# Kernel tuning notes

Measured on AMD Instinct MI355X. Metric: run time of the kernel, lower is better.

## Reference

```python
import jax, jax.numpy as jnp
import numpy as np

BETA = 0.9      # membrane decay
THRESH = 1.0    # firing threshold


def _lif(x):
    """Leaky integrate-and-fire over leading time axis. x: (T, ..., C) -> spikes (T, ..., C)."""
    def step(mem, xt):
        mem = BETA * mem + xt
        s = (mem > THRESH).astype(xt.dtype)
        mem = mem - s * THRESH  # soft reset
        return mem, s
    _, spikes = jax.lax.scan(step, jnp.zeros_like(x[0]), x)
    return spikes


def setup_inputs() -> dict:
    key = jax.random.key(0)
    k1, k2, k3, k4, k5 = jax.random.split(key, 5)
    T, N, D = 4, 8192, 1024
    E, EF, TOPK = 8, 512, 2  # expert_ff = d_ff // n_experts = 4096 // 8
    x = jax.random.normal(k1, (T, N, D), dtype=jnp.float32)
    expert_indices = jax.random.randint(k2, (N, TOPK), 0, E)
    expert_weights = jax.random.uniform(k3, (N, TOPK), dtype=jnp.float32)
    up_w = jax.random.normal(k4, (E, EF, D), dtype=jnp.float32) * 0.02   # Linear(d_model, ef).weight
    down_w = jax.random.normal(k5, (E, D, EF), dtype=jnp.float32) * 0.02  # Linear(ef, d_model).weight
    return {"x": x, "expert_indices": expert_indices, "expert_weights": expert_weights,
            "up_w": up_w, "down_w": down_w}


def reference(x, expert_indices, expert_weights, up_w, down_w):
    T, N, D = x.shape
    E = up_w.shape[0]
    # Dense combine weights W[n, e] = sum_k weights[n, k] * (indices[n, k] == e)
    W = jnp.zeros((N, E), dtype=x.dtype).at[
        jnp.arange(N)[:, None], expert_indices].add(expert_weights)
    out = jnp.zeros_like(x)
    for e in range(E):  # fixed small loop over experts
        h = _lif(jnp.einsum('tnd,fd->tnf', x, up_w[e]))   # up-proj + LIF hidden
        o = _lif(jnp.einsum('tnf,df->tnd', h, down_w[e]))  # down-proj + LIF output
        out = out + o * W[:, e][None, :, None]             # weighted combine (0 for inactive)
    return out
```

## Files before the change

### kernel.cpp

```cpp
#include <hip/hip_runtime.h>
#include <stdint.h>

#define T_STEPS 4
#define NTOK    8192
#define DMODEL  1024
#define NEXP    8
#define EFF     512
#define BMT     128
#define CAPTOT  (2*NTOK + NEXP*BMT)

typedef __attribute__((ext_vector_type(8))) short bf8_t;
typedef __attribute__((ext_vector_type(4))) float f32x4;

#define MFMA(a,b,c) __builtin_amdgcn_mfma_f32_16x16x32_bf16((a),(b),(c),0,0,0)

#define SWZC(r, c) ((((c) ^ (((r) >> 1) & 3))) * 8)


__device__ __forceinline__ unsigned short bf16rn(float f) {
    unsigned u = __float_as_uint(f);
    unsigned r = u + 0x7fffu + ((u >> 16) & 1u);
    return (unsigned short)(r >> 16);
}
__device__ __forceinline__ float bf2f(unsigned short h) {
    return __uint_as_float(((unsigned)h) << 16);
}
__device__ __forceinline__ unsigned pk(unsigned short a, unsigned short b) {
    return (unsigned)a | ((unsigned)b << 16);
}

__device__ __forceinline__ void split8v(float4 va, float4 vb,
                                        unsigned short* d0, unsigned short* d1,
                                        unsigned short* d2) {
    float v[8];
    *(float4*)&v[0] = va;
    *(float4*)&v[4] = vb;
    unsigned short h[8], m[8], l[8];
#pragma unroll
    for (int i = 0; i < 8; ++i) {
        unsigned short a = bf16rn(v[i]);
        float r1 = v[i] - bf2f(a);
        unsigned short b = bf16rn(r1);
        float r2 = r1 - bf2f(b);
        h[i] = a; m[i] = b; l[i] = bf16rn(r2);
    }
    *(uint4*)d0 = make_uint4(pk(h[0],h[1]), pk(h[2],h[3]), pk(h[4],h[5]), pk(h[6],h[7]));
    *(uint4*)d1 = make_uint4(pk(m[0],m[1]), pk(m[2],m[3]), pk(m[4],m[5]), pk(m[6],m[7]));
    *(uint4*)d2 = make_uint4(pk(l[0],l[1]), pk(l[2],l[3]), pk(l[4],l[5]), pk(l[6],l[7]));
}

__device__ __forceinline__ void stage8_3limb(const float* __restrict__ src,
                                             unsigned short* d0, unsigned short* d1,
                                             unsigned short* d2) {
    float4 va = *(const float4*)(src + 0);
    float4 vb = *(const float4*)(src + 4);
    split8v(va, vb, d0, d1, d2);
}


__global__ void k_split(const float* __restrict__ w, unsigned short* __restrict__ h,
                        unsigned short* __restrict__ m, unsigned short* __restrict__ l) {
    size_t i = (size_t)(blockIdx.x * blockDim.x + threadIdx.x) * 8;
    stage8_3limb(w + i, h + i, m + i, l + i);
}


__global__ void k_count(const int* __restrict__ idx, int* __restrict__ counts) {
    int n = blockIdx.x * blockDim.x + threadIdx.x;
    if (n >= NTOK) return;
    int e0 = idx[2*n], e1 = idx[2*n+1];
    atomicAdd(&counts[e0], 1);
    if (e1 != e0) atomicAdd(&counts[e1], 1);
}

__global__ void k_prefix(const int* __restrict__ counts, int* __restrict__ offsets) {
    if (threadIdx.x == 0) {
        int o = 0;
        for (int e = 0; e < NEXP; ++e) {
            offsets[e] = o;
            o += (counts[e] + BMT - 1) / BMT * BMT;
        }
        offsets[NEXP] = o;
    }
}

__global__ void k_fill(const int* __restrict__ idx, const float* __restrict__ wts,
                       const int* __restrict__ offsets, int* __restrict__ cursors,
                       int* __restrict__ tok, float* __restrict__ wgt) {
    int n = blockIdx.x * blockDim.x + threadIdx.x;
    if (n >= NTOK) return;
    int e0 = idx[2*n], e1 = idx[2*n+1];
    float w0 = wts[2*n], w1 = wts[2*n+1];
    if (e0 == e1) w0 = __fadd_rn(w0, w1);
    int p0 = offsets[e0] + atomicAdd(&cursors[e0], 1);
    tok[p0] = n; wgt[p0] = w0;
    if (e1 != e0) {
        int p1 = offsets[e1] + atomicAdd(&cursors[e1], 1);
        tok[p1] = n; wgt[p1] = w1;
    }
}


__global__ __launch_bounds__(256, 2)
void k_up(const float* __restrict__ x,
          const unsigned short* __restrict__ uwh, const unsigned short* __restrict__ uwm,
          const unsigned short* __restrict__ uwl,
          const int* __restrict__ offsets, const int* __restrict__ tok,
          unsigned short* __restrict__ spk) {
    const int m0 = blockIdx.x * BMT;
    const int ft = blockIdx.y;
    if (m0 >= offsets[NEXP]) return;
    int e = 0;
    for (int i = 1; i < NEXP; ++i) if (m0 >= offsets[i]) e = i;

    __shared__ unsigned short As[3][128][32];
    __shared__ unsigned short Bs[3][128][32];

    const int tid  = threadIdx.x;
    const int lane = tid & 63, wid = tid >> 6;
    const int quad = lane >> 4, l16 = lane & 15;
    const int mw = (wid & 1) * 64, nw = (wid >> 1) * 64;

    const int r = tid >> 1, half = tid & 1;
    const int c0 = SWZC(r, half*2 + 0);
    const int c1 = SWZC(r, half*2 + 1);
    const int tokA = tok[m0 + r];
    const float* xbase = x + (size_t)tokA * DMODEL + half * 16;
    const size_t woff = ((size_t)e * EFF + ft * 128 + r) * DMODEL + half * 16;
    const unsigned short* bhp = uwh + woff;
    const unsigned short* bmp = uwm + woff;
    const unsigned short* blp = uwl + woff;

    const int kq = SWZC(l16, quad);

    f32x4 mem[4][4];
#pragma unroll
    for (int i = 0; i < 4; ++i)
#pragma unroll
        for (int j = 0; j < 4; ++j) mem[i][j] = (f32x4){0.f,0.f,0.f,0.f};

    float4 pa[4];
#pragma unroll
    for (int i = 0; i < 4; ++i) pa[i] = ((const float4*)xbase)[i];

    for (int t = 0; t < T_STEPS; ++t) {
        f32x4 acc[4][4];
#pragma unroll
        for (int i = 0; i < 4; ++i)
#pragma unroll
            for (int j = 0; j < 4; ++j) acc[i][j] = (f32x4){0.f,0.f,0.f,0.f};

        for (int kc = 0; kc < DMODEL; kc += 32) {
            __syncthreads();
            split8v(pa[0], pa[1], &As[0][r][c0], &As[1][r][c0], &As[2][r][c0]);
            split8v(pa[2], pa[3], &As[0][r][c1], &As[1][r][c1], &As[2][r][c1]);
            *(uint4*)&Bs[0][r][c0] = *(const uint4*)(bhp + kc);
            *(uint4*)&Bs[0][r][c1] = *(const uint4*)(bhp + kc + 8);
            *(uint4*)&Bs[1][r][c0] = *(const uint4*)(bmp + kc);
            *(uint4*)&Bs[1][r][c1] = *(const uint4*)(bmp + kc + 8);
            *(uint4*)&Bs[2][r][c0] = *(const uint4*)(blp + kc);
            *(uint4*)&Bs[2][r][c1] = *(const uint4*)(blp + kc + 8);
            __syncthreads();

            if (!(t == T_STEPS - 1 && kc == DMODEL - 32)) {
                const float* nxt = (kc == DMODEL - 32)
                    ? xbase + (size_t)(t + 1) * NTOK * DMODEL
                    : xbase + (size_t)t * NTOK * DMODEL + kc + 32;
#pragma unroll
                for (int i = 0; i < 4; ++i) pa[i] = ((const float4*)nxt)[i];
            }

            bf8_t bh[4], bm[4], bl[4];
#pragma unroll
            for (int nt = 0; nt < 4; ++nt) {
                const int nr = nw + nt*16 + l16;
                bh[nt] = *(const bf8_t*)&Bs[0][nr][kq];
                bm[nt] = *(const bf8_t*)&Bs[1][nr][kq];
                bl[nt] = *(const bf8_t*)&Bs[2][nr][kq];
            }
#pragma unroll
            for (int mt = 0; mt < 4; ++mt) {
                const int mr = mw + mt*16 + l16;
                bf8_t ah = *(const bf8_t*)&As[0][mr][kq];
                bf8_t am = *(const bf8_t*)&As[1][mr][kq];
                bf8_t al = *(const bf8_t*)&As[2][mr][kq];
#pragma unroll
                for (int nt = 0; nt < 4; ++nt) {
                    f32x4 c = acc[mt][nt];
                    c = MFMA(ah, bh[nt], c);
                    c = MFMA(am, bh[nt], c);
                    c = MFMA(ah, bm[nt], c);
                    c = MFMA(am, bm[nt], c);
                    c = MFMA(al, bh[nt], c);
                    c = MFMA(ah, bl[nt], c);
                    acc[mt][nt] = c;
                }
            }
        }

#pragma unroll
        for (int mt = 0; mt < 4; ++mt)
#pragma unroll
            for (int nt = 0; nt < 4; ++nt)
#pragma unroll
                for (int reg = 0; reg < 4; ++reg) {
                    float mv = __fadd_rn(__fmul_rn(0.9f, mem[mt][nt][reg]), acc[mt][nt][reg]);
                    bool s = mv > 1.0f;
                    mem[mt][nt][reg] = __fsub_rn(mv, s ? 1.0f : 0.0f);
                    int row = m0 + mw + mt*16 + quad*4 + reg;
                    int col = ft*128 + nw + nt*16 + l16;
                    spk[((size_t)t * CAPTOT + row) * EFF + col] = s ? 0x3F80u : 0u;
                }
    }
}


__global__ __launch_bounds__(256, 2)
void k_dn(const unsigned short* __restrict__ spk,
          const unsigned short* __restrict__ dwh, const unsigned short* __restrict__ dwm,
          const unsigned short* __restrict__ dwl,
          const int* __restrict__ offsets, const int* __restrict__ tok,
          const float* __restrict__ wgt, float* __restrict__ out) {
    const int m0 = blockIdx.x * BMT;
    const int dt = blockIdx.y;
    if (m0 >= offsets[NEXP]) return;
    int e = 0;
    for (int i = 1; i < NEXP; ++i) if (m0 >= offsets[i]) e = i;

    __shared__ unsigned short As[128][32];
    __shared__ unsigned short Bs[3][128][32];

    const int tid  = threadIdx.x;
    const int lane = tid & 63, wid = tid >> 6;
    const int quad = lane >> 4, l16 = lane & 15;
    const int mw = (wid & 1) * 64, nw = (wid >> 1) * 64;

    const int r = tid >> 1, half = tid & 1;
    const int c0 = SWZC(r, half*2 + 0);
    const int c1 = SWZC(r, half*2 + 1);
    const unsigned short* arow = spk + (size_t)(m0 + r) * EFF + half * 16;
    const size_t doff = ((size_t)e * DMODEL + dt * 128 + r) * EFF + half * 16;
    const unsigned short* bhp = dwh + doff;
    const unsigned short* bmp = dwm + doff;
    const unsigned short* blp = dwl + doff;

    const int kq = SWZC(l16, quad);

    f32x4 mem[4][4];
#pragma unroll
    for (int i = 0; i < 4; ++i)
#pragma unroll
        for (int j = 0; j < 4; ++j) mem[i][j] = (f32x4){0.f,0.f,0.f,0.f};

    uint4 pa0 = *(const uint4*)(arow + 0);
    uint4 pa1 = *(const uint4*)(arow + 8);

    for (int t = 0; t < T_STEPS; ++t) {
        f32x4 acc[4][4];
#pragma unroll
        for (int i = 0; i < 4; ++i)
#pragma unroll
            for (int j = 0; j < 4; ++j) acc[i][j] = (f32x4){0.f,0.f,0.f,0.f};

        for (int kc = 0; kc < EFF; kc += 32) {
            __syncthreads();
            *(uint4*)&As[r][c0] = pa0;
            *(uint4*)&As[r][c1] = pa1;
            *(uint4*)&Bs[0][r][c0] = *(const uint4*)(bhp + kc);
            *(uint4*)&Bs[0][r][c1] = *(const uint4*)(bhp + kc + 8);
            *(uint4*)&Bs[1][r][c0] = *(const uint4*)(bmp + kc);
            *(uint4*)&Bs[1][r][c1] = *(const uint4*)(bmp + kc + 8);
            *(uint4*)&Bs[2][r][c0] = *(const uint4*)(blp + kc);
            *(uint4*)&Bs[2][r][c1] = *(const uint4*)(blp + kc + 8);
            __syncthreads();

            if (!(t == T_STEPS - 1 && kc == EFF - 32)) {
                const unsigned short* nxt = (kc == EFF - 32)
                    ? arow + (size_t)(t + 1) * CAPTOT * EFF
                    : arow + (size_t)t * CAPTOT * EFF + kc + 32;
                pa0 = *(const uint4*)(nxt + 0);
                pa1 = *(const uint4*)(nxt + 8);
            }

            bf8_t bh[4], bm[4], bl[4];
#pragma unroll
            for (int nt = 0; nt < 4; ++nt) {
                const int nr = nw + nt*16 + l16;
                bh[nt] = *(const bf8_t*)&Bs[0][nr][kq];
                bm[nt] = *(const bf8_t*)&Bs[1][nr][kq];
                bl[nt] = *(const bf8_t*)&Bs[2][nr][kq];
            }
#pragma unroll
            for (int mt = 0; mt < 4; ++mt) {
                const int mr = mw + mt*16 + l16;
                bf8_t a = *(const bf8_t*)&As[mr][kq];
#pragma unroll
                for (int nt = 0; nt < 4; ++nt) {
                    f32x4 c = acc[mt][nt];
                    c = MFMA(a, bh[nt], c);
                    c = MFMA(a, bm[nt], c);
                    c = MFMA(a, bl[nt], c);
                    acc[mt][nt] = c;
                }
            }
        }

#pragma unroll
        for (int mt = 0; mt < 4; ++mt) {
            const int rbase = m0 + mw + mt*16 + quad*4;
#pragma unroll
            for (int reg = 0; reg < 4; ++reg) {
                const int   n = tok[rbase + reg];
                const float w = wgt[rbase + reg];
#pragma unroll
                for (int nt = 0; nt < 4; ++nt) {
                    float mv = __fadd_rn(__fmul_rn(0.9f, mem[mt][nt][reg]), acc[mt][nt][reg]);
                    bool s = mv > 1.0f;
                    mem[mt][nt][reg] = __fsub_rn(mv, s ? 1.0f : 0.0f);
                    if (s && w != 0.0f) {
                        int col = dt*128 + nw + nt*16 + l16;
                        atomicAdd(out + ((size_t)t * NTOK + n) * DMODEL + col, w);
                    }
                }
            }
        }
    }
}


extern "C" void kernel_launch(void* const* d_in, const int* in_sizes, int n_in,
                              void* d_out, int out_size, void* d_ws, size_t ws_size,
                              hipStream_t stream) {
    const float* x      = (const float*)d_in[0];
    const int*   idx    = (const int*)  d_in[1];
    const float* wts    = (const float*)d_in[2];
    const float* up_w   = (const float*)d_in[3];
    const float* down_w = (const float*)d_in[4];
    float* out = (float*)d_out;

    char* ws = (char*)d_ws;
    int*   counts  = (int*)(ws + 0);
    int*   cursors = (int*)(ws + 32);
    int*   offsets = (int*)(ws + 64);
    int*   tok     = (int*)(ws + 128);
    float* wgt     = (float*)(ws + 128 + (size_t)CAPTOT * 4);
    unsigned short* spk = (unsigned short*)(ws + 128 + (size_t)CAPTOT * 8);

    const size_t WSPK = (size_t)T_STEPS * CAPTOT * EFF * 2;
    size_t base2 = 128 + (size_t)CAPTOT * 8 + WSPK;
    base2 = (base2 + 511) & ~(size_t)511;
    const size_t WLIMB = (size_t)NEXP * EFF * DMODEL * 2;
    unsigned short* uwh = (unsigned short*)(ws + base2);
    unsigned short* uwm = (unsigned short*)(ws + base2 + 1*WLIMB);
    unsigned short* uwl = (unsigned short*)(ws + base2 + 2*WLIMB);
    unsigned short* dwh = (unsigned short*)(ws + base2 + 3*WLIMB);
    unsigned short* dwm = (unsigned short*)(ws + base2 + 4*WLIMB);
    unsigned short* dwl = (unsigned short*)(ws + base2 + 5*WLIMB);

    hipMemsetAsync(ws, 0, 128 + (size_t)CAPTOT * 8, stream);
    hipMemsetAsync(out, 0, (size_t)out_size * sizeof(float), stream);

    const int nsplit = NEXP * EFF * DMODEL / 8 / 256;
    k_split<<<nsplit, 256, 0, stream>>>(up_w,   uwh, uwm, uwl);
    k_split<<<nsplit, 256, 0, stream>>>(down_w, dwh, dwm, dwl);

    k_count <<<(NTOK + 255) / 256, 256, 0, stream>>>(idx, counts);
    k_prefix<<<1, 64, 0, stream>>>(counts, offsets);
    k_fill  <<<(NTOK + 255) / 256, 256, 0, stream>>>(idx, wts, offsets, cursors, tok, wgt);

    dim3 gup(CAPTOT / BMT, EFF / 128);
    k_up<<<gup, 256, 0, stream>>>(x, uwh, uwm, uwl, offsets, tok, spk);

    dim3 gdn(CAPTOT / BMT, DMODEL / 128);
    k_dn<<<gdn, 256, 0, stream>>>(spk, dwh, dwm, dwl, offsets, tok, wgt, out);
}
```

Baseline: 987.9 us.

## Double-buffer weight and spike tiles via direct global-to-LDS DMA loads

Both up and down kernels now load B (weight limbs) and, in the down kernel, the A spike tiles straight from global memory into LDS with global_load_lds. The tiles are double-buffered so the next k-slice is fetched while MFMAs run on the current one, with manual waitcnt and barrier control. The DMA lane-to-column mapping is meant to reproduce the existing XOR swizzle. This targets the register round-trip and the load latency that sat on the critical path between barriers. In exchange it doubles LDS use and relies on hand-counted vmcnt values, which could break correctness or occupancy if the counts are wrong.

```diff
diff --git a/kernel.cpp b/kernel.cpp
--- a/kernel.cpp
+++ b/kernel.cpp
@@ -15,6 +15,14 @@
 #define MFMA(a,b,c) __builtin_amdgcn_mfma_f32_16x16x32_bf16((a),(b),(c),0,0,0)
 
 #define SWZC(r, c) ((((c) ^ (((r) >> 1) & 3))) * 8)
+
+typedef __attribute__((address_space(3))) unsigned int lds_uint;
+typedef const __attribute__((address_space(1))) unsigned int glb_uint;
+__device__ __forceinline__ void dma16(const void* g, void* l) {
+    __builtin_amdgcn_global_load_lds((glb_uint*)g, (lds_uint*)l, 16, 0, 0);
+}
+#define S_BARRIER() __builtin_amdgcn_s_barrier()
+#define SFENCE()    __builtin_amdgcn_sched_barrier(0)
 
 
 __device__ __forceinline__ unsigned short bf16rn(float f) {
@@ -113,8 +121,8 @@
     int e = 0;
     for (int i = 1; i < NEXP; ++i) if (m0 >= offsets[i]) e = i;
 
-    __shared__ unsigned short As[3][128][32];
-    __shared__ unsigned short Bs[3][128][32];
+    __shared__ __align__(16) unsigned short As[3][128][32];
+    __shared__ __align__(16) unsigned short Bs[2][3][128][32];
 
     const int tid  = threadIdx.x;
     const int lane = tid & 63, wid = tid >> 6;
@@ -126,10 +134,11 @@
     const int c1 = SWZC(r, half*2 + 1);
     const int tokA = tok[m0 + r];
     const float* xbase = x + (size_t)tokA * DMODEL + half * 16;
-    const size_t woff = ((size_t)e * EFF + ft * 128 + r) * DMODEL + half * 16;
-    const unsigned short* bhp = uwh + woff;
-    const unsigned short* bmp = uwm + woff;
-    const unsigned short* blp = uwl + woff;
+
+    const unsigned short* wlimb[3] = { uwh, uwm, uwl };
+    const size_t wrow0 = ((size_t)e * EFF + ft * 128) * DMODEL;
+    const int drow  = lane >> 2;
+    const int dclog = (lane & 3) ^ ((lane >> 3) & 3);
 
     const int kq = SWZC(l16, quad);
 
@@ -139,10 +148,17 @@
 #pragma unroll
         for (int j = 0; j < 4; ++j) mem[i][j] = (f32x4){0.f,0.f,0.f,0.f};
 
+#pragma unroll
+    for (int j = 0; j < 6; ++j) {
+        const int limb = j >> 1, rh = j & 1;
+        dma16(wlimb[limb] + wrow0 + (size_t)(rh*64 + wid*16 + drow) * DMODEL + dclog*8,
+              &Bs[0][limb][rh*64 + wid*16][0]);
+    }
     float4 pa[4];
 #pragma unroll
     for (int i = 0; i < 4; ++i) pa[i] = ((const float4*)xbase)[i];
 
+    int cur = 0;
     for (int t = 0; t < T_STEPS; ++t) {
         f32x4 acc[4][4];
 #pragma unroll
@@ -150,33 +166,47 @@
 #pragma unroll
             for (int j = 0; j < 4; ++j) acc[i][j] = (f32x4){0.f,0.f,0.f,0.f};
 
+        const float* xrow = xbase + (size_t)t * NTOK * DMODEL;
+
         for (int kc = 0; kc < DMODEL; kc += 32) {
-            __syncthreads();
+            const bool last = (t == T_STEPS - 1) && (kc == DMODEL - 32);
+            asm volatile("s_waitcnt lgkmcnt(0)" ::: "memory");
+            SFENCE();
+            S_BARRIER();
+            SFENCE();
+            if (!last) {
+                const int nkk = (kc == DMODEL - 32) ? 0 : kc + 32;
+#pragma unroll
+                for (int j = 0; j < 6; ++j) {
+                    const int limb = j >> 1, rh = j & 1;
+                    dma16(wlimb[limb] + wrow0 + (size_t)(rh*64 + wid*16 + drow) * DMODEL
+                              + nkk + dclog*8,
+                          &Bs[cur ^ 1][limb][rh*64 + wid*16][0]);
+                }
+            }
             split8v(pa[0], pa[1], &As[0][r][c0], &As[1][r][c0], &As[2][r][c0]);
             split8v(pa[2], pa[3], &As[0][r][c1], &As[1][r][c1], &As[2][r][c1]);
-            *(uint4*)&Bs[0][r][c0] = *(const uint4*)(bhp + kc);
-            *(uint4*)&Bs[0][r][c1] = *(const uint4*)(bhp + kc + 8);
-            *(uint4*)&Bs[1][r][c0] = *(const uint4*)(bmp + kc);
-            *(uint4*)&Bs[1][r][c1] = *(const uint4*)(bmp + kc + 8);
-            *(uint4*)&Bs[2][r][c0] = *(const uint4*)(blp + kc);
-            *(uint4*)&Bs[2][r][c1] = *(const uint4*)(blp + kc + 8);
-            __syncthreads();
-
-            if (!(t == T_STEPS - 1 && kc == DMODEL - 32)) {
-                const float* nxt = (kc == DMODEL - 32)
+            if (!last) {
+                const float* nxtA = (kc == DMODEL - 32)
                     ? xbase + (size_t)(t + 1) * NTOK * DMODEL
-                    : xbase + (size_t)t * NTOK * DMODEL + kc + 32;
-#pragma unroll
-                for (int i = 0; i < 4; ++i) pa[i] = ((const float4*)nxt)[i];
-            }
+                    : xrow + kc + 32;
+#pragma unroll
+                for (int i = 0; i < 4; ++i) pa[i] = ((const float4*)nxtA)[i];
+                asm volatile("s_waitcnt vmcnt(10) lgkmcnt(0)" ::: "memory");
+            } else {
+                asm volatile("s_waitcnt vmcnt(0) lgkmcnt(0)" ::: "memory");
+            }
+            SFENCE();
+            S_BARRIER();
+            SFENCE();
 
             bf8_t bh[4], bm[4], bl[4];
 #pragma unroll
             for (int nt = 0; nt < 4; ++nt) {
                 const int nr = nw + nt*16 + l16;
-                bh[nt] = *(const bf8_t*)&Bs[0][nr][kq];
-                bm[nt] = *(const bf8_t*)&Bs[1][nr][kq];
-                bl[nt] = *(const bf8_t*)&Bs[2][nr][kq];
+                bh[nt] = *(const bf8_t*)&Bs[cur][0][nr][kq];
+                bm[nt] = *(const bf8_t*)&Bs[cur][1][nr][kq];
+                bl[nt] = *(const bf8_t*)&Bs[cur][2][nr][kq];
             }
 #pragma unroll
             for (int mt = 0; mt < 4; ++mt) {
@@ -196,6 +226,7 @@
                     acc[mt][nt] = c;
                 }
             }
+            cur ^= 1;
         }
 
 #pragma unroll
@@ -227,22 +258,18 @@
     int e = 0;
     for (int i = 1; i < NEXP; ++i) if (m0 >= offsets[i]) e = i;
 
-    __shared__ unsigned short As[128][32];
-    __shared__ unsigned short Bs[3][128][32];
+    __shared__ __align__(16) unsigned short As[2][128][32];
+    __shared__ __align__(16) unsigned short Bs[2][3][128][32];
 
     const int tid  = threadIdx.x;
     const int lane = tid & 63, wid = tid >> 6;
     const int quad = lane >> 4, l16 = lane & 15;
     const int mw = (wid & 1) * 64, nw = (wid >> 1) * 64;
 
-    const int r = tid >> 1, half = tid & 1;
-    const int c0 = SWZC(r, half*2 + 0);
-    const int c1 = SWZC(r, half*2 + 1);
-    const unsigned short* arow = spk + (size_t)(m0 + r) * EFF + half * 16;
-    const size_t doff = ((size_t)e * DMODEL + dt * 128 + r) * EFF + half * 16;
-    const unsigned short* bhp = dwh + doff;
-    const unsigned short* bmp = dwm + doff;
-    const unsigned short* blp = dwl + doff;
+    const unsigned short* dlimb[3] = { dwh, dwm, dwl };
+    const size_t drow0 = ((size_t)e * DMODEL + dt * 128) * EFF;
+    const int drow  = lane >> 2;
+    const int dclog = (lane & 3) ^ ((lane >> 3) & 3);
 
     const int kq = SWZC(l16, quad);
 
@@ -252,9 +279,20 @@
 #pragma unroll
         for (int j = 0; j < 4; ++j) mem[i][j] = (f32x4){0.f,0.f,0.f,0.f};
 
-    uint4 pa0 = *(const uint4*)(arow + 0);
-    uint4 pa1 = *(const uint4*)(arow + 8);
-
+#pragma unroll
+    for (int j2 = 0; j2 < 2; ++j2) {
+        const int row = j2*64 + wid*16 + drow;
+        dma16(spk + ((size_t)0 * CAPTOT + m0 + row) * EFF + dclog*8,
+              &As[0][j2*64 + wid*16][0]);
+    }
+#pragma unroll
+    for (int j = 0; j < 6; ++j) {
+        const int limb = j >> 1, rh = j & 1;
+        dma16(dlimb[limb] + drow0 + (size_t)(rh*64 + wid*16 + drow) * EFF + dclog*8,
+              &Bs[0][limb][rh*64 + wid*16][0]);
+    }
+
+    int cur = 0;
     for (int t = 0; t < T_STEPS; ++t) {
         f32x4 acc[4][4];
 #pragma unroll
@@ -263,37 +301,47 @@
             for (int j = 0; j < 4; ++j) acc[i][j] = (f32x4){0.f,0.f,0.f,0.f};
 
         for (int kc = 0; kc < EFF; kc += 32) {
-            __syncthreads();
-            *(uint4*)&As[r][c0] = pa0;
-            *(uint4*)&As[r][c1] = pa1;
-            *(uint4*)&Bs[0][r][c0] = *(const uint4*)(bhp + kc);
-            *(uint4*)&Bs[0][r][c1] = *(const uint4*)(bhp + kc + 8);
-            *(uint4*)&Bs[1][r][c0] = *(const uint4*)(bmp + kc);
-            *(uint4*)&Bs[1][r][c1] = *(const uint4*)(bmp + kc + 8);
-            *(uint4*)&Bs[2][r][c0] = *(const uint4*)(blp + kc);
-            *(uint4*)&Bs[2][r][c1] = *(const uint4*)(blp + kc + 8);
-            __syncthreads();
-
-            if (!(t == T_STEPS - 1 && kc == EFF - 32)) {
-                const unsigned short* nxt = (kc == EFF - 32)
-                    ? arow + (size_t)(t + 1) * CAPTOT * EFF
-                    : arow + (size_t)t * CAPTOT * EFF + kc + 32;
-                pa0 = *(const uint4*)(nxt + 0);
-                pa1 = *(const uint4*)(nxt + 8);
-            }
+            const bool last = (t == T_STEPS - 1) && (kc == EFF - 32);
+            asm volatile("s_waitcnt lgkmcnt(0)" ::: "memory");
+            SFENCE();
+            S_BARRIER();
+            SFENCE();
+            if (!last) {
+                int ntt = t, nkk = kc + 32;
+                if (nkk == EFF) { nkk = 0; ntt = t + 1; }
+#pragma unroll
+                for (int j2 = 0; j2 < 2; ++j2) {
+                    const int row = j2*64 + wid*16 + drow;
+                    dma16(spk + ((size_t)ntt * CAPTOT + m0 + row) * EFF + nkk + dclog*8,
+                          &As[cur ^ 1][j2*64 + wid*16][0]);
+                }
+#pragma unroll
+                for (int j = 0; j < 6; ++j) {
+                    const int limb = j >> 1, rh = j & 1;
+                    dma16(dlimb[limb] + drow0 + (size_t)(rh*64 + wid*16 + drow) * EFF
+                              + nkk + dclog*8,
+                          &Bs[cur ^ 1][limb][rh*64 + wid*16][0]);
+                }
+                asm volatile("s_waitcnt vmcnt(8)" ::: "memory");
+            } else {
+                asm volatile("s_waitcnt vmcnt(0)" ::: "memory");
+            }
+            SFENCE();
+            S_BARRIER();
+            SFENCE();
 
             bf8_t bh[4], bm[4], bl[4];
 #pragma unroll
             for (int nt = 0; nt < 4; ++nt) {
                 const int nr = nw + nt*16 + l16;
-                bh[nt] = *(const bf8_t*)&Bs[0][nr][kq];
-                bm[nt] = *(const bf8_t*)&Bs[1][nr][kq];
-                bl[nt] = *(const bf8_t*)&Bs[2][nr][kq];
+                bh[nt] = *(const bf8_t*)&Bs[cur][0][nr][kq];
+                bm[nt] = *(const bf8_t*)&Bs[cur][1][nr][kq];
+                bl[nt] = *(const bf8_t*)&Bs[cur][2][nr][kq];
             }
 #pragma unroll
             for (int mt = 0; mt < 4; ++mt) {
                 const int mr = mw + mt*16 + l16;
-                bf8_t a = *(const bf8_t*)&As[mr][kq];
+                bf8_t a = *(const bf8_t*)&As[cur][mr][kq];
 #pragma unroll
                 for (int nt = 0; nt < 4; ++nt) {
                     f32x4 c = acc[mt][nt];
@@ -303,6 +351,7 @@
                     acc[mt][nt] = c;
                 }
             }
+            cur ^= 1;
         }
 
 #pragma unroll
```

After: 960.1 us. 2.8% less time.
